# Kernel tuning notes

Measured on AMD Instinct MI355X. Metric: run time of the kernel, lower is better.

The kernel has to match this reference:

```python
import jax, jax.numpy as jnp
import numpy as np

NEG_SLOPE = 0.2


def gat_conv(x, edge_index, W, att_src, att_dst, bias, heads, out_ch):
    """PyG GATConv (add_self_loops=True, concat=True) in jax.
    x: [N, F_in], edge_index: [2, E] (row0=src j, row1=dst i).
    Returns [N, heads*out_ch].
    """
    N = x.shape[0]
    # add self loops (PyG default)
    loops = jnp.tile(jnp.arange(N, dtype=edge_index.dtype)[None, :], (2, 1))
    ei = jnp.concatenate([edge_index, loops], axis=1)
    src, dst = ei[0], ei[1]
    h = (x @ W).reshape(N, heads, out_ch)              # [N,H,C]
    a_src = (h * att_src).sum(-1)                      # [N,H]
    a_dst = (h * att_dst).sum(-1)                      # [N,H]
    alpha = jax.nn.leaky_relu(a_src[src] + a_dst[dst], NEG_SLOPE)  # [E,H]
    # segment softmax over destination nodes
    amax = jax.ops.segment_max(alpha, dst, num_segments=N)         # [N,H]
    ealpha = jnp.exp(alpha - amax[dst])
    denom = jax.ops.segment_sum(ealpha, dst, num_segments=N)
    alpha = ealpha / jnp.maximum(denom, 1e-16)[dst]
    msg = h[src] * alpha[..., None]                    # [E,H,C]
    out = jax.ops.segment_sum(msg, dst, num_segments=N)  # [N,H,C]
    return out.reshape(N, heads * out_ch) + bias


def setup_inputs() -> dict:
    key = jax.random.key(0)
    ks = jax.random.split(key, 16)
    N, F_in, E, E_lab, Fe = 10000, 128, 160000, 100000, 16
    H1, C = 4, 128  # gat1 heads, hidden_dim
    inp = {
        "x": jax.random.normal(ks[0], (N, F_in), jnp.float32),
        "edge_index": jax.random.randint(ks[1], (2, E), 0, N, jnp.int64),
        "edge_attr": jax.random.normal(ks[2], (E, Fe), jnp.float32),
        "edge_label_index": jax.random.randint(ks[3], (2, E_lab), 0, N, jnp.int64),
        "edge_label_attr": jax.random.normal(ks[4], (E_lab, Fe), jnp.float32),
        # gat1 params
        "W1": jax.random.normal(ks[5], (F_in, H1 * C), jnp.float32) / np.sqrt(F_in),
        "att_src1": jax.random.normal(ks[6], (1, H1, C), jnp.float32) / np.sqrt(C),
        "att_dst1": jax.random.normal(ks[7], (1, H1, C), jnp.float32) / np.sqrt(C),
        "b1": jnp.zeros((H1 * C,), jnp.float32),
        # gat2 params (heads=1)
        "W2": jax.random.normal(ks[8], (H1 * C, C), jnp.float32) / np.sqrt(H1 * C),
        "att_src2": jax.random.normal(ks[9], (1, 1, C), jnp.float32) / np.sqrt(C),
        "att_dst2": jax.random.normal(ks[10], (1, 1, C), jnp.float32) / np.sqrt(C),
        "b2": jnp.zeros((C,), jnp.float32),
        # edge MLP: actual input dim = C + Fe = 144 (see notes)
        "mlp_w1": jax.random.normal(ks[11], (C + Fe, 64), jnp.float32) / np.sqrt(C + Fe),
        "mlp_b1": jnp.zeros((64,), jnp.float32),
        "mlp_w2": jax.random.normal(ks[12], (64, 2), jnp.float32) / np.sqrt(64.0),
        "mlp_b2": jnp.zeros((2,), jnp.float32),
    }
    return inp


def reference(x, edge_index, edge_attr, edge_label_index, edge_label_attr,
              W1, att_src1, att_dst1, b1, W2, att_src2, att_dst2, b2,
              mlp_w1, mlp_b1, mlp_w2, mlp_b2):
    # edge_attr is unused by the original forward (GATConv called without it)
    h = jax.nn.elu(gat_conv(x, edge_index, W1, att_src1, att_dst1, b1, heads=4, out_ch=128))
    h = jax.nn.elu(gat_conv(h, edge_index, W2, att_src2, att_dst2, b2, heads=1, out_ch=128))
    edge_src = h[edge_label_index[0]]
    edge_dst = h[edge_label_index[1]]
    edge_emb = edge_src * edge_dst                     # [E_lab, 128]
    feats = jnp.concatenate([edge_emb, edge_label_attr], axis=1)
    out = jax.nn.relu(feats @ mlp_w1 + mlp_b1) @ mlp_w2 + mlp_b2
    return out
```

## Files before the change

### kernel.cpp

```cpp
#include <hip/hip_runtime.h>
#include <hip/hip_bf16.h>
#include <cstdint>

typedef __attribute__((ext_vector_type(8))) short bf16x8;
typedef __attribute__((ext_vector_type(4))) float f32x4;

__device__ __forceinline__ float lrelu02(float x){ return x > 0.f ? x : 0.2f*x; }
__device__ __forceinline__ float elu1(float x){ return x > 0.f ? x : __expf(x)-1.f; }
__device__ __forceinline__ unsigned short bf16_rne(float f){
  unsigned int u = __float_as_uint(f);
  u += 0x7FFFu + ((u >> 16) & 1u);
  return (unsigned short)(u >> 16);
}
__device__ __forceinline__ float b2f(unsigned int hi16){ return __uint_as_float(hi16 << 16); }
__device__ __forceinline__ unsigned int packbf(float a, float b){
  return (unsigned int)bf16_rne(a) | ((unsigned int)bf16_rne(b) << 16);
}

__device__ __forceinline__ float wave_reduce_sum(float v){
  #pragma unroll
  for (int o = 32; o >= 1; o >>= 1) v += __shfl_xor(v, o, 64);
  return v;
}

__global__ void hist_kernel(const int* __restrict__ ei, int* __restrict__ cnt, int E){
  int e = blockIdx.x*blockDim.x + threadIdx.x;
  if (e < E) atomicAdd(&cnt[ei[E + e]], 1);
}

__global__ void scan_kernel(const int* __restrict__ cnt, int* __restrict__ rp, int N){
  __shared__ int part[1024];
  const int PER = 16;
  int t = threadIdx.x;
  int base = t*PER;
  int local[PER]; int s = 0;
  #pragma unroll
  for (int i=0;i<PER;i++){ int idx=base+i; int v = (idx<N)? cnt[idx] : 0; local[i]=s; s+=v; }
  part[t]=s; __syncthreads();
  for (int off=1; off<1024; off<<=1){
    int v = (t>=off)? part[t-off] : 0;
    __syncthreads();
    part[t] += v;
    __syncthreads();
  }
  int ex = (t>0)? part[t-1] : 0;
  #pragma unroll
  for (int i=0;i<PER;i++){ int idx=base+i; if (idx<N) rp[idx] = ex + local[i]; }
  if (t==0) rp[N] = part[1023];
}

__global__ void fill_kernel(const int* __restrict__ ei, const int* __restrict__ rp,
                            int* __restrict__ fl, int* __restrict__ col, int E){
  int e = blockIdx.x*blockDim.x + threadIdx.x;
  if (e >= E) return;
  int d = ei[E+e];
  int pos = rp[d] + atomicAdd(&fl[d], 1);
  col[pos] = ei[e];
}

__global__ void conv_all_kernel(const float* __restrict__ x, unsigned short* __restrict__ xb,
                                const float* __restrict__ W1, unsigned short* __restrict__ W1t,
                                const float* __restrict__ W2, unsigned short* __restrict__ W2t,
                                const float* __restrict__ mw1, unsigned short* __restrict__ mw1t,
                                int* __restrict__ zbase, int nz){
  int t = blockIdx.x*256 + threadIdx.x;
  if (t < 320000){
    int i = t*4;
    float4 v = *(const float4*)(x + i);
    xb[i+0] = bf16_rne(v.x); xb[i+1] = bf16_rne(v.y);
    xb[i+2] = bf16_rne(v.z); xb[i+3] = bf16_rne(v.w);
  } else if (t < 385536){
    int i = t - 320000;
    int n = i >> 7, k = i & 127;
    W1t[i] = bf16_rne(W1[(size_t)k*512 + n]);
  } else if (t < 451072){
    int i = t - 385536;
    int n = i >> 9, k = i & 511;
    W2t[i] = bf16_rne(W2[(size_t)k*128 + n]);
  } else if (t < 461312){
    int i = t - 451072;
    int n = i / 160, k = i % 160;
    mw1t[i] = (k < 144) ? bf16_rne(mw1[(size_t)k*64 + n]) : (unsigned short)0;
  } else if (t < 461312 + nz){
    zbase[t - 461312] = 0;
  }
}

template<int BN, int SPLITK, int RELU, int WB, int OUTB>
__global__ __launch_bounds__(256) void mgemm_kernel(
    const unsigned short* __restrict__ A,
    const unsigned short* __restrict__ Bt,
    const float* __restrict__ bias,
    void* __restrict__ C,
    int M, int N, int K){
  const int BM = 128, BK = 32, LDP = BK + 8;
  const int NF = BN/32;
  __shared__ unsigned short As[BM*LDP];
  __shared__ unsigned short Bs[BN*LDP];
  int tid = threadIdx.x;
  int lane = tid & 63, wid = tid >> 6;
  int wr = wid >> 1, wc = wid & 1;
  int row0 = blockIdx.y*BM, col0 = blockIdx.x*BN;
  int kchunk = K / SPLITK;
  int k0base = blockIdx.z * kchunk;
  f32x4 acc[4][NF];
  #pragma unroll
  for (int m=0;m<4;m++)
    #pragma unroll
    for (int n=0;n<NF;n++) acc[m][n] = (f32x4){0.f,0.f,0.f,0.f};

  for (int kt = 0; kt < kchunk; kt += BK){
    int k0 = k0base + kt;
    #pragma unroll
    for (int i=0;i<(BM*4)/256;i++){
      int li = i*256 + tid;
      int r = li >> 2, q = li & 3;
      int gr = row0 + r;
      uint4 v = make_uint4(0u,0u,0u,0u);
      if (gr < M) v = *(const uint4*)(A + (size_t)gr*K + k0 + q*8);
      *(uint4*)(&As[r*LDP + q*8]) = v;
    }
    #pragma unroll
    for (int i=0;i<(BN*4)/256;i++){
      int li = i*256 + tid;
      int r = li >> 2, q = li & 3;
      int gn = col0 + r;
      uint4 v = make_uint4(0u,0u,0u,0u);
      if (gn < N) v = *(const uint4*)(Bt + (size_t)gn*K + k0 + q*8);
      *(uint4*)(&Bs[r*LDP + q*8]) = v;
    }
    __syncthreads();
    int kq = (lane >> 4) * 8;
    bf16x8 af[4], bfr[NF];
    #pragma unroll
    for (int m=0;m<4;m++)
      af[m] = *(const bf16x8*)(&As[(wr*64 + m*16 + (lane&15))*LDP + kq]);
    #pragma unroll
    for (int n=0;n<NF;n++)
      bfr[n] = *(const bf16x8*)(&Bs[(wc*(BN/2) + n*16 + (lane&15))*LDP + kq]);
    #pragma unroll
    for (int m=0;m<4;m++)
      #pragma unroll
      for (int n=0;n<NF;n++)
        acc[m][n] = __builtin_amdgcn_mfma_f32_16x16x32_bf16(af[m], bfr[n], acc[m][n], 0, 0, 0);
    __syncthreads();
  }
  #pragma unroll
  for (int m=0;m<4;m++){
    #pragma unroll
    for (int j=0;j<4;j++){
      int r = row0 + wr*64 + m*16 + (lane>>4)*4 + j;
      if (r >= M) continue;
      #pragma unroll
      for (int n=0;n<NF;n++){
        int c = col0 + wc*(BN/2) + n*16 + (lane&15);
        float v = acc[m][n][j];
        if (WB) v += bias[c];
        if (RELU) v = fmaxf(v, 0.f);
        if (OUTB){
          ((unsigned short*)C)[(size_t)r*N + c] = bf16_rne(v);
        } else {
          float* Cb = (float*)C + (size_t)blockIdx.z * M * N;
          Cb[(size_t)r*N + c] = v;
        }
      }
    }
  }
}

__global__ __launch_bounds__(256) void mgemm_mlp2_kernel(
    const unsigned short* __restrict__ hf,
    const int* __restrict__ eli,
    const float* __restrict__ attr,
    const unsigned short* __restrict__ Bt,
    const float* __restrict__ mb1,
    const float* __restrict__ w2,
    const float* __restrict__ b2,
    float* __restrict__ out, int M){
  const int BK = 32, LDP = BK + 8, K = 160;
  __shared__ unsigned short As[128*LDP];
  __shared__ unsigned short Bs[64*LDP];
  __shared__ float hid[128][65];
  __shared__ float w2s[128];
  int tid = threadIdx.x;
  int lane = tid & 63, wid = tid >> 6;
  int wr = wid >> 1, wc = wid & 1;
  int row0 = blockIdx.y*128;
  if (tid < 128) w2s[tid] = w2[tid];

  int r0_ = tid >> 2, q_ = tid & 3;
  int r1_ = 64 + r0_;
  int gr0 = row0 + r0_, gr1 = row0 + r1_;
  bool ok0 = gr0 < M, ok1 = gr1 < M;
  int s0=0, d0=0, s1=0, d1=0;
  if (ok0){ s0 = eli[gr0]; d0 = eli[M + gr0]; }
  if (ok1){ s1 = eli[gr1]; d1 = eli[M + gr1]; }

  auto make_chunk = [&](int s, int d, int gr, bool ok, int k) -> uint4 {
    uint4 v = make_uint4(0u,0u,0u,0u);
    if (!ok) return v;
    if (k < 128){
      uint4 a = *(const uint4*)(hf + (size_t)s*128 + k);
      uint4 b = *(const uint4*)(hf + (size_t)d*128 + k);
      v.x = packbf(b2f(a.x & 0xffffu)*b2f(b.x & 0xffffu), b2f(a.x >> 16)*b2f(b.x >> 16));
      v.y = packbf(b2f(a.y & 0xffffu)*b2f(b.y & 0xffffu), b2f(a.y >> 16)*b2f(b.y >> 16));
      v.z = packbf(b2f(a.z & 0xffffu)*b2f(b.z & 0xffffu), b2f(a.z >> 16)*b2f(b.z >> 16));
      v.w = packbf(b2f(a.w & 0xffffu)*b2f(b.w & 0xffffu), b2f(a.w >> 16)*b2f(b.w >> 16));
    } else if (k < 144){
      const float* pa = attr + (size_t)gr*16 + (k - 128);
      float4 x0 = *(const float4*)pa;
      float4 x1 = *(const float4*)(pa + 4);
      v.x = packbf(x0.x, x0.y); v.y = packbf(x0.z, x0.w);
      v.z = packbf(x1.x, x1.y); v.w = packbf(x1.z, x1.w);
    }
    return v;
  };

  f32x4 acc[4][2];
  #pragma unroll
  for (int m=0;m<4;m++){ acc[m][0] = (f32x4){0,0,0,0}; acc[m][1] = (f32x4){0,0,0,0}; }

  for (int k0 = 0; k0 < K; k0 += BK){
    int k = k0 + q_*8;
    *(uint4*)(&As[r0_*LDP + q_*8]) = make_chunk(s0, d0, gr0, ok0, k);
    *(uint4*)(&As[r1_*LDP + q_*8]) = make_chunk(s1, d1, gr1, ok1, k);
    {
      int r = tid >> 2, q = tid & 3;
      uint4 v = *(const uint4*)(Bt + (size_t)r*K + k0 + q*8);
      *(uint4*)(&Bs[r*LDP + q*8]) = v;
    }
    __syncthreads();
    int kq = (lane >> 4) * 8;
    bf16x8 af[4], bfr[2];
    #pragma unroll
    for (int m=0;m<4;m++)
      af[m] = *(const bf16x8*)(&As[(wr*64 + m*16 + (lane&15))*LDP + kq]);
    #pragma unroll
    for (int n=0;n<2;n++)
      bfr[n] = *(const bf16x8*)(&Bs[(wc*32 + n*16 + (lane&15))*LDP + kq]);
    #pragma unroll
    for (int m=0;m<4;m++)
      #pragma unroll
      for (int n=0;n<2;n++)
        acc[m][n] = __builtin_amdgcn_mfma_f32_16x16x32_bf16(af[m], bfr[n], acc[m][n], 0, 0, 0);
    __syncthreads();
  }
  #pragma unroll
  for (int m=0;m<4;m++){
    #pragma unroll
    for (int j=0;j<4;j++){
      int r = wr*64 + m*16 + (lane>>4)*4 + j;
      #pragma unroll
      for (int n=0;n<2;n++){
        int c = wc*32 + n*16 + (lane&15);
        hid[r][c] = fmaxf(acc[m][n][j] + mb1[c], 0.f);
      }
    }
  }
  __syncthreads();
  int r = tid >> 1, hf2 = tid & 1;
  int cbase = hf2*32;
  float p0 = 0.f, p1 = 0.f;
  #pragma unroll
  for (int c=0;c<32;c++){
    float v = hid[r][cbase + c];
    p0 += v * w2s[(cbase + c)*2 + 0];
    p1 += v * w2s[(cbase + c)*2 + 1];
  }
  p0 += __shfl_xor(p0, 1, 64);
  p1 += __shfl_xor(p1, 1, 64);
  if (hf2 == 0 && row0 + r < M){
    out[(size_t)(row0 + r)*2 + 0] = p0 + b2[0];
    out[(size_t)(row0 + r)*2 + 1] = p1 + b2[1];
  }
}

__global__ void reduce4b_attn_kernel(const float4* __restrict__ p, uint2* __restrict__ o,
                                     const float* __restrict__ as2, const float* __restrict__ ad2,
                                     float* __restrict__ asrc, float* __restrict__ adst,
                                     int N, int s4){
  int idx = blockIdx.x*256 + threadIdx.x;
  int n = idx >> 5;
  if (n >= N) return;
  float4 a = p[idx], b = p[idx+s4], c = p[idx+2*s4], d = p[idx+3*s4];
  float rx = a.x+b.x+c.x+d.x, ry = a.y+b.y+c.y+d.y;
  float rz = a.z+b.z+c.z+d.z, rw = a.w+b.w+c.w+d.w;
  o[idx] = make_uint2(packbf(rx, ry), packbf(rz, rw));
  int c4 = (idx & 31)*4;
  float ps = rx*as2[c4] + ry*as2[c4+1] + rz*as2[c4+2] + rw*as2[c4+3];
  float pd = rx*ad2[c4] + ry*ad2[c4+1] + rz*ad2[c4+2] + rw*ad2[c4+3];
  #pragma unroll
  for (int off=1; off<32; off<<=1){ ps += __shfl_xor(ps,off,64); pd += __shfl_xor(pd,off,64); }
  if ((idx & 31) == 0){ asrc[n] = ps; adst[n] = pd; }
}

__global__ void attn4_kernel(const unsigned short* __restrict__ h,
                             const float* __restrict__ att_src,
                             const float* __restrict__ att_dst,
                             float* __restrict__ asrc, float* __restrict__ adst, int N){
  int lane = threadIdx.x & 63;
  int n = blockIdx.x*4 + (threadIdx.x >> 6);
  if (n >= N) return;
  const uint4* hp = (const uint4*)(h + (size_t)n*512);
  uint4 u = hp[lane];
  int ch = lane*8;
  float f0 = b2f(u.x & 0xffffu), f1 = b2f(u.x >> 16);
  float f2 = b2f(u.y & 0xffffu), f3 = b2f(u.y >> 16);
  float f4 = b2f(u.z & 0xffffu), f5 = b2f(u.z >> 16);
  float f6 = b2f(u.w & 0xffffu), f7 = b2f(u.w >> 16);
  float s = f0*att_src[ch+0] + f1*att_src[ch+1] + f2*att_src[ch+2] + f3*att_src[ch+3]
          + f4*att_src[ch+4] + f5*att_src[ch+5] + f6*att_src[ch+6] + f7*att_src[ch+7];
  float d = f0*att_dst[ch+0] + f1*att_dst[ch+1] + f2*att_dst[ch+2] + f3*att_dst[ch+3]
          + f4*att_dst[ch+4] + f5*att_dst[ch+5] + f6*att_dst[ch+6] + f7*att_dst[ch+7];
  #pragma unroll
  for (int o=1; o<16; o<<=1){ s += __shfl_xor(s, o, 64); d += __shfl_xor(d, o, 64); }
  if ((lane & 15) == 0){
    int hh = lane >> 4;
    asrc[n*4 + hh] = s; adst[n*4 + hh] = d;
  }
}

__global__ void agg4_kernel(const unsigned short* __restrict__ h,
                            const float* __restrict__ asrc,
                            const float* __restrict__ adst,
                            const float* __restrict__ bias,
                            const int* __restrict__ rp,
                            const int* __restrict__ col,
                            unsigned short* __restrict__ outb, int N){
  int lane = threadIdx.x & 63;
  int n = blockIdx.x*4 + (threadIdx.x >> 6);
  if (n >= N) return;
  int hh = lane >> 4;
  int beg = rp[n], end = rp[n+1];
  float adst_i = adst[n*4 + hh];
  float wself = __expf(lrelu02(asrc[n*4 + hh] + adst_i));
  const uint4* hp = (const uint4*)(h + (size_t)n*512);
  uint4 us = hp[lane];
  float a0 = b2f(us.x & 0xffffu)*wself, a1 = b2f(us.x >> 16)*wself;
  float a2 = b2f(us.y & 0xffffu)*wself, a3 = b2f(us.y >> 16)*wself;
  float a4 = b2f(us.z & 0xffffu)*wself, a5 = b2f(us.z >> 16)*wself;
  float a6 = b2f(us.w & 0xffffu)*wself, a7 = b2f(us.w >> 16)*wself;
  float wsum = wself;

  int e = beg;
  for (; e + 8 <= end; e += 8){
    int s0 = col[e],   s1 = col[e+1], s2 = col[e+2], s3 = col[e+3];
    int s4 = col[e+4], s5 = col[e+5], s6 = col[e+6], s7 = col[e+7];
    uint4 u0 = ((const uint4*)(h + (size_t)s0*512))[lane];
    uint4 u1 = ((const uint4*)(h + (size_t)s1*512))[lane];
    uint4 u2 = ((const uint4*)(h + (size_t)s2*512))[lane];
    uint4 u3 = ((const uint4*)(h + (size_t)s3*512))[lane];
    uint4 u4 = ((const uint4*)(h + (size_t)s4*512))[lane];
    uint4 u5 = ((const uint4*)(h + (size_t)s5*512))[lane];
    uint4 u6 = ((const uint4*)(h + (size_t)s6*512))[lane];
    uint4 u7 = ((const uint4*)(h + (size_t)s7*512))[lane];
    float w0 = __expf(lrelu02(asrc[s0*4 + hh] + adst_i));
    float w1 = __expf(lrelu02(asrc[s1*4 + hh] + adst_i));
    float w2 = __expf(lrelu02(asrc[s2*4 + hh] + adst_i));
    float w3 = __expf(lrelu02(asrc[s3*4 + hh] + adst_i));
    float w4 = __expf(lrelu02(asrc[s4*4 + hh] + adst_i));
    float w5 = __expf(lrelu02(asrc[s5*4 + hh] + adst_i));
    float w6 = __expf(lrelu02(asrc[s6*4 + hh] + adst_i));
    float w7 = __expf(lrelu02(asrc[s7*4 + hh] + adst_i));
    wsum += w0 + w1 + w2 + w3 + w4 + w5 + w6 + w7;
    a0 += b2f(u0.x & 0xffffu)*w0; a1 += b2f(u0.x >> 16)*w0;
    a2 += b2f(u0.y & 0xffffu)*w0; a3 += b2f(u0.y >> 16)*w0;
    a4 += b2f(u0.z & 0xffffu)*w0; a5 += b2f(u0.z >> 16)*w0;
    a6 += b2f(u0.w & 0xffffu)*w0; a7 += b2f(u0.w >> 16)*w0;
    a0 += b2f(u1.x & 0xffffu)*w1; a1 += b2f(u1.x >> 16)*w1;
    a2 += b2f(u1.y & 0xffffu)*w1; a3 += b2f(u1.y >> 16)*w1;
    a4 += b2f(u1.z & 0xffffu)*w1; a5 += b2f(u1.z >> 16)*w1;
    a6 += b2f(u1.w & 0xffffu)*w1; a7 += b2f(u1.w >> 16)*w1;
    a0 += b2f(u2.x & 0xffffu)*w2; a1 += b2f(u2.x >> 16)*w2;
    a2 += b2f(u2.y & 0xffffu)*w2; a3 += b2f(u2.y >> 16)*w2;
    a4 += b2f(u2.z & 0xffffu)*w2; a5 += b2f(u2.z >> 16)*w2;
    a6 += b2f(u2.w & 0xffffu)*w2; a7 += b2f(u2.w >> 16)*w2;
    a0 += b2f(u3.x & 0xffffu)*w3; a1 += b2f(u3.x >> 16)*w3;
    a2 += b2f(u3.y & 0xffffu)*w3; a3 += b2f(u3.y >> 16)*w3;
    a4 += b2f(u3.z & 0xffffu)*w3; a5 += b2f(u3.z >> 16)*w3;
    a6 += b2f(u3.w & 0xffffu)*w3; a7 += b2f(u3.w >> 16)*w3;
    a0 += b2f(u4.x & 0xffffu)*w4; a1 += b2f(u4.x >> 16)*w4;
    a2 += b2f(u4.y & 0xffffu)*w4; a3 += b2f(u4.y >> 16)*w4;
    a4 += b2f(u4.z & 0xffffu)*w4; a5 += b2f(u4.z >> 16)*w4;
    a6 += b2f(u4.w & 0xffffu)*w4; a7 += b2f(u4.w >> 16)*w4;
    a0 += b2f(u5.x & 0xffffu)*w5; a1 += b2f(u5.x >> 16)*w5;
    a2 += b2f(u5.y & 0xffffu)*w5; a3 += b2f(u5.y >> 16)*w5;
    a4 += b2f(u5.z & 0xffffu)*w5; a5 += b2f(u5.z >> 16)*w5;
    a6 += b2f(u5.w & 0xffffu)*w5; a7 += b2f(u5.w >> 16)*w5;
    a0 += b2f(u6.x & 0xffffu)*w6; a1 += b2f(u6.x >> 16)*w6;
    a2 += b2f(u6.y & 0xffffu)*w6; a3 += b2f(u6.y >> 16)*w6;
    a4 += b2f(u6.z & 0xffffu)*w6; a5 += b2f(u6.z >> 16)*w6;
    a6 += b2f(u6.w & 0xffffu)*w6; a7 += b2f(u6.w >> 16)*w6;
    a0 += b2f(u7.x & 0xffffu)*w7; a1 += b2f(u7.x >> 16)*w7;
    a2 += b2f(u7.y & 0xffffu)*w7; a3 += b2f(u7.y >> 16)*w7;
    a4 += b2f(u7.z & 0xffffu)*w7; a5 += b2f(u7.z >> 16)*w7;
    a6 += b2f(u7.w & 0xffffu)*w7; a7 += b2f(u7.w >> 16)*w7;
  }
  for (; e + 4 <= end; e += 4){
    int s0 = col[e], s1 = col[e+1], s2 = col[e+2], s3 = col[e+3];
    uint4 u0 = ((const uint4*)(h + (size_t)s0*512))[lane];
    uint4 u1 = ((const uint4*)(h + (size_t)s1*512))[lane];
    uint4 u2 = ((const uint4*)(h + (size_t)s2*512))[lane];
    uint4 u3 = ((const uint4*)(h + (size_t)s3*512))[lane];
    float w0 = __expf(lrelu02(asrc[s0*4 + hh] + adst_i));
    float w1 = __expf(lrelu02(asrc[s1*4 + hh] + adst_i));
    float w2 = __expf(lrelu02(asrc[s2*4 + hh] + adst_i));
    float w3 = __expf(lrelu02(asrc[s3*4 + hh] + adst_i));
    wsum += w0 + w1 + w2 + w3;
    a0 += b2f(u0.x & 0xffffu)*w0; a1 += b2f(u0.x >> 16)*w0;
    a2 += b2f(u0.y & 0xffffu)*w0; a3 += b2f(u0.y >> 16)*w0;
    a4 += b2f(u0.z & 0xffffu)*w0; a5 += b2f(u0.z >> 16)*w0;
    a6 += b2f(u0.w & 0xffffu)*w0; a7 += b2f(u0.w >> 16)*w0;
    a0 += b2f(u1.x & 0xffffu)*w1; a1 += b2f(u1.x >> 16)*w1;
    a2 += b2f(u1.y & 0xffffu)*w1; a3 += b2f(u1.y >> 16)*w1;
    a4 += b2f(u1.z & 0xffffu)*w1; a5 += b2f(u1.z >> 16)*w1;
    a6 += b2f(u1.w & 0xffffu)*w1; a7 += b2f(u1.w >> 16)*w1;
    a0 += b2f(u2.x & 0xffffu)*w2; a1 += b2f(u2.x >> 16)*w2;
    a2 += b2f(u2.y & 0xffffu)*w2; a3 += b2f(u2.y >> 16)*w2;
    a4 += b2f(u2.z & 0xffffu)*w2; a5 += b2f(u2.z >> 16)*w2;
    a6 += b2f(u2.w & 0xffffu)*w2; a7 += b2f(u2.w >> 16)*w2;
    a0 += b2f(u3.x & 0xffffu)*w3; a1 += b2f(u3.x >> 16)*w3;
    a2 += b2f(u3.y & 0xffffu)*w3; a3 += b2f(u3.y >> 16)*w3;
    a4 += b2f(u3.z & 0xffffu)*w3; a5 += b2f(u3.z >> 16)*w3;
    a6 += b2f(u3.w & 0xffffu)*w3; a7 += b2f(u3.w >> 16)*w3;
  }
  for (; e < end; ++e){
    int s0 = col[e];
    uint4 u0 = ((const uint4*)(h + (size_t)s0*512))[lane];
    float w0 = __expf(lrelu02(asrc[s0*4 + hh] + adst_i));
    wsum += w0;
    a0 += b2f(u0.x & 0xffffu)*w0; a1 += b2f(u0.x >> 16)*w0;
    a2 += b2f(u0.y & 0xffffu)*w0; a3 += b2f(u0.y >> 16)*w0;
    a4 += b2f(u0.z & 0xffffu)*w0; a5 += b2f(u0.z >> 16)*w0;
    a6 += b2f(u0.w & 0xffffu)*w0; a7 += b2f(u0.w >> 16)*w0;
  }
  float inv = 1.f / fmaxf(wsum, 1e-16f);
  int ch = lane*8;
  float o0 = elu1(a0*inv + bias[ch+0]);
  float o1 = elu1(a1*inv + bias[ch+1]);
  float o2 = elu1(a2*inv + bias[ch+2]);
  float o3 = elu1(a3*inv + bias[ch+3]);
  float o4 = elu1(a4*inv + bias[ch+4]);
  float o5 = elu1(a5*inv + bias[ch+5]);
  float o6 = elu1(a6*inv + bias[ch+6]);
  float o7 = elu1(a7*inv + bias[ch+7]);
  ((uint4*)(outb + (size_t)n*512))[lane] =
      make_uint4(packbf(o0,o1), packbf(o2,o3), packbf(o4,o5), packbf(o6,o7));
}

__global__ void agg1_kernel(const unsigned short* __restrict__ h,
                            const float* __restrict__ asrc,
                            const float* __restrict__ adst,
                            const float* __restrict__ bias,
                            const int* __restrict__ rp,
                            const int* __restrict__ col,
                            unsigned short* __restrict__ outb, int N){
  const int C = 128;
  int lane = threadIdx.x & 63;
  int n = blockIdx.x*4 + (threadIdx.x >> 6);
  if (n >= N) return;
  int beg = rp[n], end = rp[n+1];
  float adst_i = adst[n];
  float wself = __expf(lrelu02(asrc[n] + adst_i));
  const unsigned int* hp = (const unsigned int*)(h + (size_t)n*C);
  unsigned int us = hp[lane];
  float acc0 = b2f(us & 0xffffu)*wself, acc1 = b2f(us >> 16)*wself;
  float wsum = wself;

  int e = beg;
  for (; e + 8 <= end; e += 8){
    int r0 = col[e],   r1 = col[e+1], r2 = col[e+2], r3 = col[e+3];
    int r4 = col[e+4], r5 = col[e+5], r6 = col[e+6], r7 = col[e+7];
    unsigned int u0 = ((const unsigned int*)(h + (size_t)r0*C))[lane];
    unsigned int u1 = ((const unsigned int*)(h + (size_t)r1*C))[lane];
    unsigned int u2 = ((const unsigned int*)(h + (size_t)r2*C))[lane];
    unsigned int u3 = ((const unsigned int*)(h + (size_t)r3*C))[lane];
    unsigned int u4 = ((const unsigned int*)(h + (size_t)r4*C))[lane];
    unsigned int u5 = ((const unsigned int*)(h + (size_t)r5*C))[lane];
    unsigned int u6 = ((const unsigned int*)(h + (size_t)r6*C))[lane];
    unsigned int u7 = ((const unsigned int*)(h + (size_t)r7*C))[lane];
    float w0 = __expf(lrelu02(asrc[r0] + adst_i));
    float w1 = __expf(lrelu02(asrc[r1] + adst_i));
    float w2 = __expf(lrelu02(asrc[r2] + adst_i));
    float w3 = __expf(lrelu02(asrc[r3] + adst_i));
    float w4 = __expf(lrelu02(asrc[r4] + adst_i));
    float w5 = __expf(lrelu02(asrc[r5] + adst_i));
    float w6 = __expf(lrelu02(asrc[r6] + adst_i));
    float w7 = __expf(lrelu02(asrc[r7] + adst_i));
    wsum += w0 + w1 + w2 + w3 + w4 + w5 + w6 + w7;
    acc0 += b2f(u0 & 0xffffu)*w0; acc1 += b2f(u0 >> 16)*w0;
    acc0 += b2f(u1 & 0xffffu)*w1; acc1 += b2f(u1 >> 16)*w1;
    acc0 += b2f(u2 & 0xffffu)*w2; acc1 += b2f(u2 >> 16)*w2;
    acc0 += b2f(u3 & 0xffffu)*w3; acc1 += b2f(u3 >> 16)*w3;
    acc0 += b2f(u4 & 0xffffu)*w4; acc1 += b2f(u4 >> 16)*w4;
    acc0 += b2f(u5 & 0xffffu)*w5; acc1 += b2f(u5 >> 16)*w5;
    acc0 += b2f(u6 & 0xffffu)*w6; acc1 += b2f(u6 >> 16)*w6;
    acc0 += b2f(u7 & 0xffffu)*w7; acc1 += b2f(u7 >> 16)*w7;
  }
  for (; e + 4 <= end; e += 4){
    int r0 = col[e], r1 = col[e+1], r2 = col[e+2], r3 = col[e+3];
    unsigned int u0 = ((const unsigned int*)(h + (size_t)r0*C))[lane];
    unsigned int u1 = ((const unsigned int*)(h + (size_t)r1*C))[lane];
    unsigned int u2 = ((const unsigned int*)(h + (size_t)r2*C))[lane];
    unsigned int u3 = ((const unsigned int*)(h + (size_t)r3*C))[lane];
    float w0 = __expf(lrelu02(asrc[r0] + adst_i));
    float w1 = __expf(lrelu02(asrc[r1] + adst_i));
    float w2 = __expf(lrelu02(asrc[r2] + adst_i));
    float w3 = __expf(lrelu02(asrc[r3] + adst_i));
    wsum += w0 + w1 + w2 + w3;
    acc0 += b2f(u0 & 0xffffu)*w0; acc1 += b2f(u0 >> 16)*w0;
    acc0 += b2f(u1 & 0xffffu)*w1; acc1 += b2f(u1 >> 16)*w1;
    acc0 += b2f(u2 & 0xffffu)*w2; acc1 += b2f(u2 >> 16)*w2;
    acc0 += b2f(u3 & 0xffffu)*w3; acc1 += b2f(u3 >> 16)*w3;
  }
  for (; e < end; ++e){
    int r0 = col[e];
    unsigned int u0 = ((const unsigned int*)(h + (size_t)r0*C))[lane];
    float w0 = __expf(lrelu02(asrc[r0] + adst_i));
    wsum += w0;
    acc0 += b2f(u0 & 0xffffu)*w0; acc1 += b2f(u0 >> 16)*w0;
  }
  float inv = 1.f / fmaxf(wsum, 1e-16f);
  int c0 = 2*lane;
  float o0 = elu1(acc0*inv + bias[c0]);
  float o1 = elu1(acc1*inv + bias[c0+1]);
  ((unsigned int*)outb)[(size_t)n*(C/2) + lane] = packbf(o0, o1);
}

extern "C" void kernel_launch(void* const* d_in, const int* in_sizes, int n_in,
                              void* d_out, int out_size, void* d_ws, size_t ws_size,
                              hipStream_t stream){
  const float* x    = (const float*)d_in[0];
  const int*   ei   = (const int*)d_in[1];
  const int*   eli  = (const int*)d_in[3];
  const float* attr = (const float*)d_in[4];
  const float* W1   = (const float*)d_in[5];
  const float* as1  = (const float*)d_in[6];
  const float* ad1  = (const float*)d_in[7];
  const float* b1   = (const float*)d_in[8];
  const float* W2   = (const float*)d_in[9];
  const float* as2  = (const float*)d_in[10];
  const float* ad2  = (const float*)d_in[11];
  const float* b2   = (const float*)d_in[12];
  const float* mw1  = (const float*)d_in[13];
  const float* mb1  = (const float*)d_in[14];
  const float* mw2  = (const float*)d_in[15];
  const float* mb2  = (const float*)d_in[16];
  float* out = (float*)d_out;

  const int N  = in_sizes[0]/128;
  const int E  = in_sizes[1]/2;
  const int EL = in_sizes[3]/2;
  const int H1 = 4, C = 128;
  const int K1 = 128, N1 = 512;
  const int K2 = 512, N2 = 128;
  const int N3 = 64, K3 = 160;
  (void)N3; (void)K3;

  char* ws = (char*)d_ws;
  auto al = [](size_t x){ return (x + 255) & ~(size_t)255; };
  size_t off = 0;
  unsigned short* W1t  = (unsigned short*)(ws + off); off += al((size_t)N1*K1*2);
  unsigned short* W2t  = (unsigned short*)(ws + off); off += al((size_t)N2*K2*2);
  unsigned short* mw1t = (unsigned short*)(ws + off); off += al((size_t)64*160*2);
  float* asrc1 = (float*)(ws + off); off += al((size_t)N*H1*4);
  float* adst1 = (float*)(ws + off); off += al((size_t)N*H1*4);
  float* asrc2 = (float*)(ws + off); off += al((size_t)N*4);
  float* adst2 = (float*)(ws + off); off += al((size_t)N*4);
  int* cnt = (int*)(ws + off); off += (size_t)N*4;
  int* fl  = (int*)(ws + off); off += al((size_t)N*4);
  int* rp  = (int*)(ws + off); off += al((size_t)(N+1)*4);
  int* col = (int*)(ws + off); off += al((size_t)E*4);
  unsigned short* out2b = (unsigned short*)(ws + off); off += al((size_t)N*C*2);
  size_t A0 = off;
  unsigned short* xb    = (unsigned short*)(ws + A0);
  unsigned short* h1    = (unsigned short*)(ws + A0 + al((size_t)N*K1*2));
  unsigned short* out1b = (unsigned short*)((char*)h1 + al((size_t)N*N1*2));
  float*          part  = (float*)((char*)out1b + al((size_t)N*N1*2));
  unsigned short* h2b   = (unsigned short*)((char*)part + al((size_t)4*N*N2*4));

  const int NZ = 2*N;
  conv_all_kernel<<<(461312 + NZ + 255)/256, 256, 0, stream>>>(
      x, xb, W1, W1t, W2, W2t, mw1, mw1t, cnt, NZ);

  hist_kernel<<<(E+255)/256, 256, 0, stream>>>(ei, cnt, E);
  scan_kernel<<<1, 1024, 0, stream>>>(cnt, rp, N);
  fill_kernel<<<(E+255)/256, 256, 0, stream>>>(ei, rp, fl, col, E);

  mgemm_kernel<64,1,0,0,1><<<dim3(N1/64, (N+127)/128, 1), 256, 0, stream>>>(
      xb, W1t, nullptr, h1, N, N1, K1);
  attn4_kernel<<<(N+3)/4, 256, 0, stream>>>(h1, as1, ad1, asrc1, adst1, N);
  agg4_kernel<<<(N+3)/4, 256, 0, stream>>>(h1, asrc1, adst1, b1, rp, col, out1b, N);

  mgemm_kernel<64,4,0,0,0><<<dim3(N2/64, (N+127)/128, 4), 256, 0, stream>>>(
      out1b, W2t, nullptr, part, N, N2, K2);
  reduce4b_attn_kernel<<<(N*32+255)/256, 256, 0, stream>>>(
      (const float4*)part, (uint2*)h2b, as2, ad2, asrc2, adst2, N, N*N2/4);
  agg1_kernel<<<(N+3)/4, 256, 0, stream>>>(h2b, asrc2, adst2, b2, rp, col, out2b, N);

  mgemm_mlp2_kernel<<<dim3(1, (EL+127)/128, 1), 256, 0, stream>>>(
      out2b, eli, attr, mw1t, mb1, mw2, mb2, out, EL);
}
```

Before: 124.5 us.

## Fuse CSR histogram, scan and fill into one cooperative kernel

Replaces the three CSR-building kernels (histogram, single-block scan, fill) with one cooperative-launch kernel of 512 blocks that uses grid-wide syncs between phases. The scan now runs in block 0 with 256 threads handling 40 entries each, instead of 1024 threads handling 16. The aim is to remove two kernel launch gaps. In exchange it pays for two grid barriers and a serial scan in one block while the other blocks wait, and it assumes N is at most 10240.

```diff
diff --git a/kernel.cpp b/kernel.cpp
--- a/kernel.cpp
+++ b/kernel.cpp
@@ -1,6 +1,9 @@
 #include <hip/hip_runtime.h>
 #include <hip/hip_bf16.h>
+#include <hip/hip_cooperative_groups.h>
 #include <cstdint>
+
+namespace cg = cooperative_groups;
 
 typedef __attribute__((ext_vector_type(8))) short bf16x8;
 typedef __attribute__((ext_vector_type(4))) float f32x4;
@@ -17,45 +20,40 @@
   return (unsigned int)bf16_rne(a) | ((unsigned int)bf16_rne(b) << 16);
 }
 
-__device__ __forceinline__ float wave_reduce_sum(float v){
-  #pragma unroll
-  for (int o = 32; o >= 1; o >>= 1) v += __shfl_xor(v, o, 64);
-  return v;
-}
-
-__global__ void hist_kernel(const int* __restrict__ ei, int* __restrict__ cnt, int E){
-  int e = blockIdx.x*blockDim.x + threadIdx.x;
-  if (e < E) atomicAdd(&cnt[ei[E + e]], 1);
-}
-
-__global__ void scan_kernel(const int* __restrict__ cnt, int* __restrict__ rp, int N){
-  __shared__ int part[1024];
-  const int PER = 16;
-  int t = threadIdx.x;
-  int base = t*PER;
-  int local[PER]; int s = 0;
-  #pragma unroll
-  for (int i=0;i<PER;i++){ int idx=base+i; int v = (idx<N)? cnt[idx] : 0; local[i]=s; s+=v; }
-  part[t]=s; __syncthreads();
-  for (int off=1; off<1024; off<<=1){
-    int v = (t>=off)? part[t-off] : 0;
-    __syncthreads();
-    part[t] += v;
-    __syncthreads();
-  }
-  int ex = (t>0)? part[t-1] : 0;
-  #pragma unroll
-  for (int i=0;i<PER;i++){ int idx=base+i; if (idx<N) rp[idx] = ex + local[i]; }
-  if (t==0) rp[N] = part[1023];
-}
-
-__global__ void fill_kernel(const int* __restrict__ ei, const int* __restrict__ rp,
-                            int* __restrict__ fl, int* __restrict__ col, int E){
-  int e = blockIdx.x*blockDim.x + threadIdx.x;
-  if (e >= E) return;
-  int d = ei[E+e];
-  int pos = rp[d] + atomicAdd(&fl[d], 1);
-  col[pos] = ei[e];
+__global__ void csr_kernel(const int* __restrict__ ei, int* __restrict__ cnt,
+                           int* __restrict__ rp, int* __restrict__ fl,
+                           int* __restrict__ col, int E, int N){
+  cg::grid_group grid = cg::this_grid();
+  int tid = blockIdx.x*blockDim.x + threadIdx.x;
+  int nth = gridDim.x*blockDim.x;
+  for (int e = tid; e < E; e += nth) atomicAdd(&cnt[ei[E + e]], 1);
+  grid.sync();
+  if (blockIdx.x == 0){
+    __shared__ int part[256];
+    const int PER = 40;
+    int t = threadIdx.x;
+    int base = t*PER;
+    int local[PER]; int s = 0;
+    #pragma unroll
+    for (int i=0;i<PER;i++){ int idx=base+i; int v = (idx<N)? cnt[idx] : 0; local[i]=s; s+=v; }
+    part[t]=s; __syncthreads();
+    for (int off=1; off<256; off<<=1){
+      int v = (t>=off)? part[t-off] : 0;
+      __syncthreads();
+      part[t] += v;
+      __syncthreads();
+    }
+    int ex = (t>0)? part[t-1] : 0;
+    #pragma unroll
+    for (int i=0;i<PER;i++){ int idx=base+i; if (idx<N) rp[idx] = ex + local[i]; }
+    if (t==0) rp[N] = part[255];
+  }
+  grid.sync();
+  for (int e = tid; e < E; e += nth){
+    int d = ei[E + e];
+    int pos = rp[d] + atomicAdd(&fl[d], 1);
+    col[pos] = ei[e];
+  }
 }
 
 __global__ void conv_all_kernel(const float* __restrict__ x, unsigned short* __restrict__ xb,
@@ -554,8 +552,6 @@
   const int H1 = 4, C = 128;
   const int K1 = 128, N1 = 512;
   const int K2 = 512, N2 = 128;
-  const int N3 = 64, K3 = 160;
-  (void)N3; (void)K3;
 
   char* ws = (char*)d_ws;
   auto al = [](size_t x){ return (x + 255) & ~(size_t)255; };
@@ -583,9 +579,14 @@
   conv_all_kernel<<<(461312 + NZ + 255)/256, 256, 0, stream>>>(
       x, xb, W1, W1t, W2, W2t, mw1, mw1t, cnt, NZ);
 
-  hist_kernel<<<(E+255)/256, 256, 0, stream>>>(ei, cnt, E);
-  scan_kernel<<<1, 1024, 0, stream>>>(cnt, rp, N);
-  fill_kernel<<<(E+255)/256, 256, 0, stream>>>(ei, rp, fl, col, E);
+  {
+    int E_ = E, N_ = N;
+    const int* ei_ = ei;
+    int* cnt_ = cnt; int* rp_ = rp; int* fl_ = fl; int* col_ = col;
+    void* args[] = { (void*)&ei_, (void*)&cnt_, (void*)&rp_, (void*)&fl_,
+                     (void*)&col_, (void*)&E_, (void*)&N_ };
+    hipLaunchCooperativeKernel((void*)csr_kernel, dim3(512), dim3(256), args, 0, stream);
+  }
 
   mgemm_kernel<64,1,0,0,1><<<dim3(N1/64, (N+127)/128, 1), 256, 0, stream>>>(
       xb, W1t, nullptr, h1, N, N1, K1);
```

After: 248.6 us. +99.7%, slower.
